# Optimization experiments

Hardware: AMD Instinct MI355X
Metric: run time of the kernel (lower is better)

## Reference

```python
import jax, jax.numpy as jnp
import numpy as np

B, C, T, H, W = 2, 128, 16, 64, 64
MAX_STEPS = 12
EXP = 2  # ReactionMLP expansion
LN_EPS = 1e-5


def setup_inputs() -> dict:
    key = jax.random.key(0)
    ks = jax.random.split(key, 12)
    s = 0.05
    u = jax.random.normal(ks[0], (B, C, T, H, W), jnp.float32)
    # Linear weights stored as (in, out); torch uses y = x @ W.T + b
    Wg = jax.random.normal(ks[1], (C, C), jnp.float32) * s
    bg = jnp.zeros((C,), jnp.float32)
    Wv = jax.random.normal(ks[2], (C, C), jnp.float32) * s
    bv = jnp.zeros((C,), jnp.float32)
    W1 = jax.random.normal(ks[3], (C, C * EXP), jnp.float32) * s
    b1 = jnp.zeros((C * EXP,), jnp.float32)
    W2 = jax.random.normal(ks[4], (C * EXP, C), jnp.float32) * s
    b2 = jnp.zeros((C,), jnp.float32)
    gamma = jnp.ones((C,), jnp.float32)
    beta = jnp.zeros((C,), jnp.float32)
    alpha = jnp.float32(0.1)
    log_dt = jnp.log(jnp.float32(0.1))
    return {"u": u, "Wg": Wg, "bg": bg, "Wv": Wv, "bv": bv,
            "W1": W1, "b1": b1, "W2": W2, "b2": b2,
            "gamma": gamma, "beta": beta, "alpha": alpha, "log_dt": log_dt}


def _layernorm(x, g, b):
    m = x.mean(-1, keepdims=True)
    xc = x - m
    v = (xc * xc).mean(-1, keepdims=True)
    return xc * jax.lax.rsqrt(v + LN_EPS) * g + b


def reference(u, Wg, bg, Wv, bv, W1, b1, W2, b2, gamma, beta, alpha, log_dt):
    Bv, Cv, Tv, Hv, Wd = u.shape
    N = Tv * Hv * Wd
    u_flat = u.transpose(0, 2, 3, 4, 1).reshape(Bv, N, Cv)  # (B, N, C)
    h0 = jnp.zeros((Bv, Cv), u.dtype)
    a = jax.nn.softplus(alpha)
    dt = jnp.clip(jnp.exp(log_dt), 0.01, 0.2)

    def step(carry, _):
        uf, h, u_prev = carry
        # Reaction MLP (per-position), torch GELU is erf-based
        react = jax.nn.gelu(uf @ W1 + b1, approximate=False) @ W2 + b2
        # Memory pump on pooled features
        u_pooled = uf.mean(axis=1)  # (B, C)
        h = h + jax.nn.sigmoid(u_pooled @ Wg + bg) * jnp.tanh(u_pooled @ Wv + bv)
        # use_pde=False -> diffusion term is zero
        du = react + a * h[:, None, :]
        u_new = _layernorm(uf + dt * du, gamma, beta)
        turb = jnp.abs(u_new - u_prev).mean() / (jnp.abs(u_prev).mean() + 1e-8)
        return (u_new, h, u_new), turb

    (uf, _, _), turbs = jax.lax.scan(step, (u_flat, h0, u_flat), None, length=MAX_STEPS)
    u_out = uf.reshape(Bv, Tv, Hv, Wd, Cv).transpose(0, 4, 1, 2, 3)
    return u_out, turbs.mean()
```

## Files before the change

### kernel.cpp

```cpp
#include <hip/hip_runtime.h>

#define NPOS 65536
#define NSTEPS 12

#define USTATE_OFF  0ull
#define STATS_OFF   67108864ull
#define H_OFF       (STATS_OFF + 128ull)
#define POOLED0_OFF (H_OFF + 2048ull)
#define PARTS_OFF   (POOLED0_OFF + 1024ull)
#define WS_END      (PARTS_OFF + 98304ull)
#define ZERO_BYTES  (WS_END - STATS_OFF)

#define L_W    0
#define L_Y1   16384
#define L_X    32832
#define L_POOL 36928
#define L_AH   37184
#define L_RED  37440
#define L_SCR  39488
#define L_TOT  39504
#define SMEM_BYTES (L_TOT * 4)

__device__ __forceinline__ float gelu_erf(float x) {
  return 0.5f * x * (1.0f + erff(x * 0.70710678118654752440f));
}

__global__ __launch_bounds__(256) void pool0_kernel(const float* __restrict__ u,
                                                    float* __restrict__ pooled0,
                                                    float* __restrict__ stats) {
  int bc = blockIdx.x;
  const float4* src = (const float4*)(u + (size_t)bc * NPOS);
  int t = threadIdx.x;
  float s = 0.f, sa = 0.f;
#pragma unroll 4
  for (int i = 0; i < 64; ++i) {
    float4 v = src[i * 256 + t];
    s += v.x + v.y + v.z + v.w;
    sa += fabsf(v.x) + fabsf(v.y) + fabsf(v.z) + fabsf(v.w);
  }
  for (int o = 1; o < 64; o <<= 1) { s += __shfl_xor(s, o, 64); sa += __shfl_xor(sa, o, 64); }
  __shared__ float sc[8];
  int lane = t & 63, w = t >> 6;
  if (lane == 0) { sc[w] = s; sc[4 + w] = sa; }
  __syncthreads();
  if (t == 0) {
    pooled0[bc] = sc[0] + sc[1] + sc[2] + sc[3];
    atomicAdd(&stats[0], sc[4] + sc[5] + sc[6] + sc[7]);
  }
}

template <int MODE>
__global__ __launch_bounds__(512)
void fused_step(const float* __restrict__ u_in, float* __restrict__ ustate,
                float* __restrict__ d_out,
                const float* __restrict__ gamma, const float* __restrict__ beta,
                const float* __restrict__ W1, const float* __restrict__ b1,
                const float* __restrict__ W2,
                const float* __restrict__ Wg, const float* __restrict__ bg,
                const float* __restrict__ Wv, const float* __restrict__ bv,
                const float* __restrict__ b2,
                const float* __restrict__ alpha_p, const float* __restrict__ logdt_p,
                float* __restrict__ h_g, const float* __restrict__ pooled0,
                float* __restrict__ parts, float* __restrict__ stats, int step) {
  extern __shared__ float sm[];
  float* sW   = sm + L_W;
  float* sY   = sm + L_Y1;
  float* sX   = sm + L_X;
  float* sPool = sm + L_POOL;
  float* sAh  = sm + L_AH;
  float* sRed = sm + L_RED;
  float* sScr = sm + L_SCR;

  int t = threadIdx.x;
  int bid = blockIdx.x;

  {
    int zb = (step + 2) % 3;
    for (int i = t; i < 8192; i += 512) parts[zb * 8192 + i] = 0.f;
  }
  if (t < 256) {
    float ps;
    if (MODE == 0) {
      ps = pooled0[t];
    } else {
      const float* pp = parts + (size_t)(step % 3) * 8192;
      ps = 0.f;
#pragma unroll
      for (int s = 0; s < 32; ++s) ps += pp[s * 256 + t];
    }
    sPool[t] = ps * (1.0f / 65536.0f);
  }
  __syncthreads();
  if (t < 256) {
    int bb = t >> 7, c = t & 127;
    float gi = bg[c], vi = bv[c];
    const float* pl = sPool + bb * 128;
    for (int k = 0; k < 128; ++k) {
      float pv = pl[k];
      gi = fmaf(pv, Wg[k * 128 + c], gi);
      vi = fmaf(pv, Wv[k * 128 + c], vi);
    }
    float sg = 1.0f / (1.0f + expf(-gi));
    float th = tanhf(vi);
    int hb = step & 1;
    float hn = h_g[hb * 256 + t] + sg * th;
    if (MODE < 2 && bid == 0) h_g[(hb ^ 1) * 256 + t] = hn;
    float aa = log1pf(expf(alpha_p[0]));
    sAh[t] = aa * hn + b2[c];
  }
  __syncthreads();

  float dtv = fminf(fmaxf(expf(logdt_p[0]), 0.01f), 0.2f);
  int b = bid >> 8;
  int og = t & 63, pgw = t >> 6;
  int og2 = t & 31, pg2 = t >> 5;
  int lane = t & 63, wv = t >> 6;

  float preg[4] = {0.f, 0.f, 0.f, 0.f};
  float acc_ad = 0.f, acc_au = 0.f;

  float4* sWf = (float4*)sW;
  const float4* W1f = (const float4*)W1;
  const float4* W2f = (const float4*)W2;

  for (int tt = 0; tt < 4; ++tt) {
    int pos0 = bid * 256 + tt * 64;
    int n0 = pos0 & (NPOS - 1);

    float a1[4][8];
#pragma unroll
    for (int i = 0; i < 4; ++i)
#pragma unroll
      for (int k = 0; k < 8; ++k) a1[i][k] = 0.f;

    for (int h = 0; h < 2; ++h) {
      __syncthreads();
#pragma unroll
      for (int it = 0; it < 8; ++it) {
        int idx = it * 512 + t;
        sWf[idx] = W1f[(size_t)(h * 64 + (idx >> 6)) * 64 + (idx & 63)];
      }
      if (MODE == 0) {
#pragma unroll
        for (int it = 0; it < 8; ++it) {
          int idx = it * 512 + t;
          int pp_ = idx & 63, cc = idx >> 6;
          sX[pp_ * 64 + cc] =
              u_in[(size_t)(b * 128 + h * 64 + cc) * NPOS + (size_t)(n0 + pp_)];
        }
      } else {
        float4* sXf = (float4*)sX;
        const float4* us4 = (const float4*)ustate;
#pragma unroll
        for (int it = 0; it < 2; ++it) {
          int idx = it * 512 + t;
          int pp_ = idx >> 4, c4 = idx & 15;
          sXf[pp_ * 16 + c4] = us4[(size_t)(pos0 + pp_) * 32 + h * 16 + c4];
        }
      }
      __syncthreads();
      const float4* Wc = (const float4*)sW;
      for (int cc = 0; cc < 64; ++cc) {
        float4 w = Wc[cc * 64 + og];
        float xv[8];
#pragma unroll
        for (int k = 0; k < 8; ++k) xv[k] = sX[(pgw * 8 + k) * 64 + cc];
#pragma unroll
        for (int k = 0; k < 8; ++k) {
          a1[0][k] = fmaf(w.x, xv[k], a1[0][k]);
          a1[1][k] = fmaf(w.y, xv[k], a1[1][k]);
          a1[2][k] = fmaf(w.z, xv[k], a1[2][k]);
          a1[3][k] = fmaf(w.w, xv[k], a1[3][k]);
        }
      }
    }
    {
      float bb1[4];
#pragma unroll
      for (int i = 0; i < 4; ++i) bb1[i] = b1[og * 4 + i];
#pragma unroll
      for (int k = 0; k < 8; ++k)
#pragma unroll
        for (int i = 0; i < 4; ++i)
          sY[(pgw * 8 + k) * 257 + og * 4 + i] = gelu_erf(a1[i][k] + bb1[i]);
    }

    float a2[4][4];
#pragma unroll
    for (int i = 0; i < 4; ++i)
#pragma unroll
      for (int k = 0; k < 4; ++k) a2[i][k] = 0.f;

    for (int h = 0; h < 2; ++h) {
      __syncthreads();
#pragma unroll
      for (int it = 0; it < 8; ++it) {
        int idx = it * 512 + t;
        sWf[idx] = W2f[(size_t)(h * 128 + (idx >> 5)) * 32 + (idx & 31)];
      }
      __syncthreads();
      const float4* Wc = (const float4*)sW;
      for (int cc = 0; cc < 128; ++cc) {
        float4 w = Wc[cc * 32 + og2];
        float yv[4];
#pragma unroll
        for (int k = 0; k < 4; ++k) yv[k] = sY[(pg2 * 4 + k) * 257 + h * 128 + cc];
#pragma unroll
        for (int k = 0; k < 4; ++k) {
          a2[0][k] = fmaf(w.x, yv[k], a2[0][k]);
          a2[1][k] = fmaf(w.y, yv[k], a2[1][k]);
          a2[2][k] = fmaf(w.z, yv[k], a2[2][k]);
          a2[3][k] = fmaf(w.w, yv[k], a2[3][k]);
        }
      }
    }

    int ch0 = og2 * 4;
    float ahv[4], gmv[4], btv[4];
#pragma unroll
    for (int i = 0; i < 4; ++i) {
      ahv[i] = sAh[b * 128 + ch0 + i];
      gmv[i] = gamma[ch0 + i];
      btv[i] = beta[ch0 + i];
    }
#pragma unroll
    for (int k = 0; k < 4; ++k) {
      int pos = pos0 + pg2 * 4 + k;
      int n = pos & (NPOS - 1);
      float uf[4];
      if (MODE == 0) {
#pragma unroll
        for (int i = 0; i < 4; ++i)
          uf[i] = u_in[(size_t)(b * 128 + ch0 + i) * NPOS + n];
      } else {
        float4 q = *(const float4*)(ustate + (size_t)pos * 128 + ch0);
        uf[0] = q.x; uf[1] = q.y; uf[2] = q.z; uf[3] = q.w;
      }
      float x[4], s1 = 0.f, s2 = 0.f;
#pragma unroll
      for (int i = 0; i < 4; ++i) {
        float du = a2[i][k] + ahv[i];
        x[i] = uf[i] + dtv * du;
        s1 += x[i]; s2 += x[i] * x[i];
      }
      for (int o = 1; o < 32; o <<= 1) {
        s1 += __shfl_xor(s1, o, 64);
        s2 += __shfl_xor(s2, o, 64);
      }
      float mean = s1 * (1.0f / 128.0f);
      float var = s2 * (1.0f / 128.0f) - mean * mean;
      float rstd = rsqrtf(var + 1e-5f);
      float un[4];
#pragma unroll
      for (int i = 0; i < 4; ++i) un[i] = (x[i] - mean) * rstd * gmv[i] + btv[i];
      if (MODE == 2) {
#pragma unroll
        for (int i = 0; i < 4; ++i)
          d_out[(size_t)(b * 128 + ch0 + i) * NPOS + n] = un[i];
      } else {
        *(float4*)(ustate + (size_t)pos * 128 + ch0) =
            make_float4(un[0], un[1], un[2], un[3]);
      }
#pragma unroll
      for (int i = 0; i < 4; ++i) {
        acc_ad += fabsf(un[i] - uf[i]);
        acc_au += fabsf(un[i]);
        preg[i] += un[i];
      }
    }
  }

  for (int o = 1; o < 64; o <<= 1) {
    acc_ad += __shfl_xor(acc_ad, o, 64);
    acc_au += __shfl_xor(acc_au, o, 64);
  }
  if (lane == 0) { sScr[wv] = acc_ad; sScr[8 + wv] = acc_au; }
#pragma unroll
  for (int i = 0; i < 4; ++i) sRed[t * 4 + i] = preg[i];
  __syncthreads();
  if (t == 0) {
    float ad = 0.f, au = 0.f;
#pragma unroll
    for (int w = 0; w < 8; ++w) { ad += sScr[w]; au += sScr[8 + w]; }
    atomicAdd(&stats[17 + step], ad);
    atomicAdd(&stats[1 + step], au);
  }
  if (MODE < 2 && t < 128) {
    float v = 0.f;
#pragma unroll
    for (int pg = 0; pg < 16; ++pg) v += sRed[(pg * 32 + (t >> 2)) * 4 + (t & 3)];
    atomicAdd(&parts[(size_t)((step + 1) % 3) * 8192 + (bid & 31) * 256 + b * 128 + t], v);
  }
}

__global__ void finalize_kernel(const float* __restrict__ stats, float* __restrict__ out) {
  if (threadIdx.x == 0 && blockIdx.x == 0) {
    const float inv = 1.0f / 16777216.0f;
    float tm = 0.f;
#pragma unroll
    for (int k = 1; k <= 12; ++k)
      tm += (stats[16 + k] * inv) / (stats[k - 1] * inv + 1e-8f);
    out[16777216] = tm * (1.0f / 12.0f);
  }
}

extern "C" void kernel_launch(void* const* d_in, const int* in_sizes, int n_in,
                              void* d_out, int out_size, void* d_ws, size_t ws_size,
                              hipStream_t stream) {
  const float* u     = (const float*)d_in[0];
  const float* Wg    = (const float*)d_in[1];
  const float* bg    = (const float*)d_in[2];
  const float* Wv    = (const float*)d_in[3];
  const float* bv    = (const float*)d_in[4];
  const float* W1    = (const float*)d_in[5];
  const float* b1    = (const float*)d_in[6];
  const float* W2    = (const float*)d_in[7];
  const float* b2    = (const float*)d_in[8];
  const float* gamma = (const float*)d_in[9];
  const float* beta  = (const float*)d_in[10];
  const float* alpha = (const float*)d_in[11];
  const float* logdt = (const float*)d_in[12];
  float* out = (float*)d_out;
  char* ws = (char*)d_ws;
  if (ws_size < WS_END) return;

  float* ustate  = (float*)(ws + USTATE_OFF);
  float* stats   = (float*)(ws + STATS_OFF);
  float* h_g     = (float*)(ws + H_OFF);
  float* pooled0 = (float*)(ws + POOLED0_OFF);
  float* parts   = (float*)(ws + PARTS_OFF);

  hipFuncSetAttribute(reinterpret_cast<const void*>(&fused_step<0>),
                      hipFuncAttributeMaxDynamicSharedMemorySize, SMEM_BYTES);
  hipFuncSetAttribute(reinterpret_cast<const void*>(&fused_step<1>),
                      hipFuncAttributeMaxDynamicSharedMemorySize, SMEM_BYTES);
  hipFuncSetAttribute(reinterpret_cast<const void*>(&fused_step<2>),
                      hipFuncAttributeMaxDynamicSharedMemorySize, SMEM_BYTES);

  hipMemsetAsync(ws + STATS_OFF, 0, ZERO_BYTES, stream);
  pool0_kernel<<<256, 256, 0, stream>>>(u, pooled0, stats);

  for (int step = 0; step < NSTEPS; ++step) {
    if (step == 0)
      fused_step<0><<<512, 512, SMEM_BYTES, stream>>>(
          u, ustate, out, gamma, beta, W1, b1, W2, Wg, bg, Wv, bv, b2,
          alpha, logdt, h_g, pooled0, parts, stats, step);
    else if (step == NSTEPS - 1)
      fused_step<2><<<512, 512, SMEM_BYTES, stream>>>(
          u, ustate, out, gamma, beta, W1, b1, W2, Wg, bg, Wv, bv, b2,
          alpha, logdt, h_g, pooled0, parts, stats, step);
    else
      fused_step<1><<<512, 512, SMEM_BYTES, stream>>>(
          u, ustate, out, gamma, beta, W1, b1, W2, Wg, bg, Wv, bv, b2,
          alpha, logdt, h_g, pooled0, parts, stats, step);
  }
  finalize_kernel<<<1, 64, 0, stream>>>(stats, out);
}
```

Baseline: 4.056 ms.

## Use bf16x3 split MFMA for reaction MLP with pre-packed weights

Replaces the scalar FP32 FMA matmuls with bf16 MFMA 16x16x32 instructions, splitting each FP32 operand into high and low bf16 parts and using three products to keep near-FP32 accuracy. A prep kernel packs W1/W2 into the MFMA fragment layout once per launch. The high halves are held in LDS and the low halves are read from global memory. Each wave now processes 32-position tiles independently, passing GELU outputs between lanes with shuffles instead of an LDS round-trip. Block count drops to 256, and the large LDS footprint limits occupancy.

New measurement: 6.330 ms. +56.1%, slower.

```diff
diff --git a/kernel.cpp b/kernel.cpp
--- a/kernel.cpp
+++ b/kernel.cpp
@@ -1,28 +1,82 @@
 #include <hip/hip_runtime.h>
 
+#define C_DIM 128
 #define NPOS 65536
 #define NSTEPS 12
+#define TILE_P 32
+#define FBLOCKS 256
+#define FTHREADS 512
+#define TOTAL_WAVES 2048
+#define TILES_PER_WAVE 2
+
+typedef short short8 __attribute__((ext_vector_type(8)));
+typedef float floatx4 __attribute__((ext_vector_type(4)));
 
 #define USTATE_OFF  0ull
-#define STATS_OFF   67108864ull
+#define PW_OFF      67108864ull
+#define STATS_OFF   (PW_OFF + 262144ull)
 #define H_OFF       (STATS_OFF + 128ull)
 #define POOLED0_OFF (H_OFF + 2048ull)
 #define PARTS_OFF   (POOLED0_OFF + 1024ull)
 #define WS_END      (PARTS_OFF + 98304ull)
 #define ZERO_BYTES  (WS_END - STATS_OFF)
 
-#define L_W    0
-#define L_Y1   16384
-#define L_X    32832
-#define L_POOL 36928
-#define L_AH   37184
-#define L_RED  37440
-#define L_SCR  39488
-#define L_TOT  39504
-#define SMEM_BYTES (L_TOT * 4)
-
+#define SM_PW1   0
+#define SM_PW2   65536
+#define SM_GAMMA 131072
+#define SM_BETA  131584
+#define SM_B1    132096
+#define SM_AH    133120
+#define SM_POOL  134144
+#define SM_PACC  135168
+#define SM_SCR   136192
+#define SMEM_BYTES 136320
+
+__device__ __forceinline__ unsigned short f2bf(float f) {
+  unsigned u = __builtin_bit_cast(unsigned, f);
+  u += 0x7fffu + ((u >> 16) & 1u);
+  return (unsigned short)(u >> 16);
+}
+__device__ __forceinline__ void split2(float a, float b, unsigned& hw, unsigned& lw) {
+  unsigned ha = (unsigned)f2bf(a), hb = (unsigned)f2bf(b);
+  float ra = a - __builtin_bit_cast(float, ha << 16);
+  float rb = b - __builtin_bit_cast(float, hb << 16);
+  hw = ha | (hb << 16);
+  lw = (unsigned)f2bf(ra) | ((unsigned)f2bf(rb) << 16);
+}
 __device__ __forceinline__ float gelu_erf(float x) {
   return 0.5f * x * (1.0f + erff(x * 0.70710678118654752440f));
+}
+__device__ __forceinline__ floatx4 mfma16(short8 a, short8 b, floatx4 c) {
+  return __builtin_amdgcn_mfma_f32_16x16x32_bf16(a, b, c, 0, 0, 0);
+}
+
+__global__ __launch_bounds__(256) void prep_weights(const float* __restrict__ W1,
+                                                    const float* __restrict__ W2,
+                                                    int4* __restrict__ pw) {
+  int t = blockIdx.x * 256 + threadIdx.x;
+  float v[8];
+  if (t < 4096) {
+    int f = t >> 6, l = t & 63;
+    int ct = f >> 2, kt = f & 3;
+    int row = ct * 16 + (l & 15);
+    int c = kt * 32 + (l >> 4) * 8;
+#pragma unroll
+    for (int j = 0; j < 8; ++j) v[j] = W1[(c + j) * 256 + row];
+  } else {
+    int t2 = t - 4096;
+    int f = t2 >> 6, l = t2 & 63;
+    int ct2 = f >> 3, kt2 = f & 7;
+    int row = ct2 * 16 + (l & 15);
+    int c = kt2 * 32 + (l >> 4) * 8;
+#pragma unroll
+    for (int j = 0; j < 8; ++j) v[j] = W2[(c + j) * 128 + row];
+  }
+  unsigned hw[4], lw[4];
+#pragma unroll
+  for (int jj = 0; jj < 4; ++jj) split2(v[2 * jj], v[2 * jj + 1], hw[jj], lw[jj]);
+  pw[t]        = make_int4((int)hw[0], (int)hw[1], (int)hw[2], (int)hw[3]);
+  pw[8192 + t] = make_int4((int)lw[0], (int)lw[1], (int)lw[2], (int)lw[3]);
 }
 
 __global__ __launch_bounds__(256) void pool0_kernel(const float* __restrict__ u,
@@ -50,51 +104,55 @@
 }
 
 template <int MODE>
-__global__ __launch_bounds__(512)
+__global__ __launch_bounds__(FTHREADS, 2)
 void fused_step(const float* __restrict__ u_in, float* __restrict__ ustate,
-                float* __restrict__ d_out,
+                float* __restrict__ d_out, const uint4* __restrict__ pw_g,
                 const float* __restrict__ gamma, const float* __restrict__ beta,
-                const float* __restrict__ W1, const float* __restrict__ b1,
-                const float* __restrict__ W2,
+                const float* __restrict__ b1, const float* __restrict__ b2,
                 const float* __restrict__ Wg, const float* __restrict__ bg,
                 const float* __restrict__ Wv, const float* __restrict__ bv,
-                const float* __restrict__ b2,
                 const float* __restrict__ alpha_p, const float* __restrict__ logdt_p,
                 float* __restrict__ h_g, const float* __restrict__ pooled0,
                 float* __restrict__ parts, float* __restrict__ stats, int step) {
-  extern __shared__ float sm[];
-  float* sW   = sm + L_W;
-  float* sY   = sm + L_Y1;
-  float* sX   = sm + L_X;
-  float* sPool = sm + L_POOL;
-  float* sAh  = sm + L_AH;
-  float* sRed = sm + L_RED;
-  float* sScr = sm + L_SCR;
-
-  int t = threadIdx.x;
-  int bid = blockIdx.x;
-
+  extern __shared__ char smem[];
+  uint4* s_pw    = (uint4*)(smem + SM_PW1);
+  float* s_gamma = (float*)(smem + SM_GAMMA);
+  float* s_beta  = (float*)(smem + SM_BETA);
+  float* s_b1    = (float*)(smem + SM_B1);
+  float* s_ah    = (float*)(smem + SM_AH);
+  float* s_pool  = (float*)(smem + SM_POOL);
+  float* s_pacc  = (float*)(smem + SM_PACC);
+  float* s_scr   = (float*)(smem + SM_SCR);
+
+  int tid = threadIdx.x;
+
+#pragma unroll
+  for (int i = 0; i < 16; ++i) s_pw[i * FTHREADS + tid] = pw_g[i * FTHREADS + tid];
+  if (tid < 128) { s_gamma[tid] = gamma[tid]; s_beta[tid] = beta[tid]; }
+  if (tid >= 128 && tid < 384) s_b1[tid - 128] = b1[tid - 128];
+  if (tid < 256) s_pacc[tid] = 0.f;
   {
     int zb = (step + 2) % 3;
-    for (int i = t; i < 8192; i += 512) parts[zb * 8192 + i] = 0.f;
-  }
-  if (t < 256) {
+#pragma unroll
+    for (int i = tid; i < 8192; i += FTHREADS) parts[zb * 8192 + i] = 0.f;
+  }
+  if (tid < 256) {
     float ps;
     if (MODE == 0) {
-      ps = pooled0[t];
+      ps = pooled0[tid];
     } else {
       const float* pp = parts + (size_t)(step % 3) * 8192;
       ps = 0.f;
 #pragma unroll
-      for (int s = 0; s < 32; ++s) ps += pp[s * 256 + t];
+      for (int s = 0; s < 32; ++s) ps += pp[s * 256 + tid];
     }
-    sPool[t] = ps * (1.0f / 65536.0f);
+    s_pool[tid] = ps * (1.0f / 65536.0f);
   }
   __syncthreads();
-  if (t < 256) {
-    int bb = t >> 7, c = t & 127;
+  if (tid < 256) {
+    int b = tid >> 7, c = tid & 127;
     float gi = bg[c], vi = bv[c];
-    const float* pl = sPool + bb * 128;
+    const float* pl = s_pool + b * 128;
     for (int k = 0; k < 128; ++k) {
       float pv = pl[k];
       gi = fmaf(pv, Wg[k * 128 + c], gi);
@@ -103,169 +161,186 @@
     float sg = 1.0f / (1.0f + expf(-gi));
     float th = tanhf(vi);
     int hb = step & 1;
-    float hn = h_g[hb * 256 + t] + sg * th;
-    if (MODE < 2 && bid == 0) h_g[(hb ^ 1) * 256 + t] = hn;
+    float hn = h_g[hb * 256 + tid] + sg * th;
+    if (MODE < 2 && blockIdx.x == 0) h_g[(hb ^ 1) * 256 + tid] = hn;
     float aa = log1pf(expf(alpha_p[0]));
-    sAh[t] = aa * hn + b2[c];
+    s_ah[tid] = aa * hn + b2[c];
   }
   __syncthreads();
 
   float dtv = fminf(fmaxf(expf(logdt_p[0]), 0.01f), 0.2f);
-  int b = bid >> 8;
-  int og = t & 63, pgw = t >> 6;
-  int og2 = t & 31, pg2 = t >> 5;
-  int lane = t & 63, wv = t >> 6;
-
-  float preg[4] = {0.f, 0.f, 0.f, 0.f};
+  int lane = tid & 63, wv = tid >> 6;
+  int p = lane & 15, g = lane >> 4;
+  int wid = blockIdx.x * 8 + wv;
   float acc_ad = 0.f, acc_au = 0.f;
 
-  float4* sWf = (float4*)sW;
-  const float4* W1f = (const float4*)W1;
-  const float4* W2f = (const float4*)W2;
-
-  for (int tt = 0; tt < 4; ++tt) {
-    int pos0 = bid * 256 + tt * 64;
-    int n0 = pos0 & (NPOS - 1);
-
-    float a1[4][8];
-#pragma unroll
-    for (int i = 0; i < 4; ++i)
-#pragma unroll
-      for (int k = 0; k < 8; ++k) a1[i][k] = 0.f;
-
-    for (int h = 0; h < 2; ++h) {
-      __syncthreads();
-#pragma unroll
-      for (int it = 0; it < 8; ++it) {
-        int idx = it * 512 + t;
-        sWf[idx] = W1f[(size_t)(h * 64 + (idx >> 6)) * 64 + (idx & 63)];
-      }
-      if (MODE == 0) {
-#pragma unroll
-        for (int it = 0; it < 8; ++it) {
-          int idx = it * 512 + t;
-          int pp_ = idx & 63, cc = idx >> 6;
-          sX[pp_ * 64 + cc] =
-              u_in[(size_t)(b * 128 + h * 64 + cc) * NPOS + (size_t)(n0 + pp_)];
-        }
-      } else {
-        float4* sXf = (float4*)sX;
-        const float4* us4 = (const float4*)ustate;
-#pragma unroll
-        for (int it = 0; it < 2; ++it) {
-          int idx = it * 512 + t;
-          int pp_ = idx >> 4, c4 = idx & 15;
-          sXf[pp_ * 16 + c4] = us4[(size_t)(pos0 + pp_) * 32 + h * 16 + c4];
-        }
-      }
-      __syncthreads();
-      const float4* Wc = (const float4*)sW;
-      for (int cc = 0; cc < 64; ++cc) {
-        float4 w = Wc[cc * 64 + og];
+  for (int it = 0; it < TILES_PER_WAVE; ++it) {
+    int tile = wid + it * TOTAL_WAVES;
+    int p0 = tile * TILE_P;
+    int b = p0 >> 16;
+    float preg[8][4];
+#pragma unroll
+    for (int c8 = 0; c8 < 8; ++c8)
+#pragma unroll
+      for (int r = 0; r < 4; ++r) preg[c8][r] = 0.f;
+
+#pragma unroll
+    for (int pt = 0; pt < 2; ++pt) {
+      int pos = p0 + pt * 16 + p;
+      int n = pos & (NPOS - 1);
+
+      short8 bxh[4], bxl[4];
+#pragma unroll
+      for (int kt = 0; kt < 4; ++kt) {
         float xv[8];
-#pragma unroll
-        for (int k = 0; k < 8; ++k) xv[k] = sX[(pgw * 8 + k) * 64 + cc];
-#pragma unroll
-        for (int k = 0; k < 8; ++k) {
-          a1[0][k] = fmaf(w.x, xv[k], a1[0][k]);
-          a1[1][k] = fmaf(w.y, xv[k], a1[1][k]);
-          a1[2][k] = fmaf(w.z, xv[k], a1[2][k]);
-          a1[3][k] = fmaf(w.w, xv[k], a1[3][k]);
-        }
-      }
-    }
-    {
-      float bb1[4];
-#pragma unroll
-      for (int i = 0; i < 4; ++i) bb1[i] = b1[og * 4 + i];
-#pragma unroll
-      for (int k = 0; k < 8; ++k)
-#pragma unroll
-        for (int i = 0; i < 4; ++i)
-          sY[(pgw * 8 + k) * 257 + og * 4 + i] = gelu_erf(a1[i][k] + bb1[i]);
-    }
-
-    float a2[4][4];
-#pragma unroll
-    for (int i = 0; i < 4; ++i)
-#pragma unroll
-      for (int k = 0; k < 4; ++k) a2[i][k] = 0.f;
-
-    for (int h = 0; h < 2; ++h) {
-      __syncthreads();
-#pragma unroll
-      for (int it = 0; it < 8; ++it) {
-        int idx = it * 512 + t;
-        sWf[idx] = W2f[(size_t)(h * 128 + (idx >> 5)) * 32 + (idx & 31)];
-      }
-      __syncthreads();
-      const float4* Wc = (const float4*)sW;
-      for (int cc = 0; cc < 128; ++cc) {
-        float4 w = Wc[cc * 32 + og2];
-        float yv[4];
-#pragma unroll
-        for (int k = 0; k < 4; ++k) yv[k] = sY[(pg2 * 4 + k) * 257 + h * 128 + cc];
-#pragma unroll
-        for (int k = 0; k < 4; ++k) {
-          a2[0][k] = fmaf(w.x, yv[k], a2[0][k]);
-          a2[1][k] = fmaf(w.y, yv[k], a2[1][k]);
-          a2[2][k] = fmaf(w.z, yv[k], a2[2][k]);
-          a2[3][k] = fmaf(w.w, yv[k], a2[3][k]);
-        }
-      }
-    }
-
-    int ch0 = og2 * 4;
-    float ahv[4], gmv[4], btv[4];
-#pragma unroll
-    for (int i = 0; i < 4; ++i) {
-      ahv[i] = sAh[b * 128 + ch0 + i];
-      gmv[i] = gamma[ch0 + i];
-      btv[i] = beta[ch0 + i];
-    }
-#pragma unroll
-    for (int k = 0; k < 4; ++k) {
-      int pos = pos0 + pg2 * 4 + k;
-      int n = pos & (NPOS - 1);
-      float uf[4];
-      if (MODE == 0) {
-#pragma unroll
-        for (int i = 0; i < 4; ++i)
-          uf[i] = u_in[(size_t)(b * 128 + ch0 + i) * NPOS + n];
-      } else {
-        float4 q = *(const float4*)(ustate + (size_t)pos * 128 + ch0);
-        uf[0] = q.x; uf[1] = q.y; uf[2] = q.z; uf[3] = q.w;
-      }
-      float x[4], s1 = 0.f, s2 = 0.f;
-#pragma unroll
-      for (int i = 0; i < 4; ++i) {
-        float du = a2[i][k] + ahv[i];
-        x[i] = uf[i] + dtv * du;
-        s1 += x[i]; s2 += x[i] * x[i];
-      }
-      for (int o = 1; o < 32; o <<= 1) {
-        s1 += __shfl_xor(s1, o, 64);
-        s2 += __shfl_xor(s2, o, 64);
-      }
+        if (MODE == 0) {
+          size_t base = ((size_t)(b * C_DIM + kt * 32 + g * 8)) * NPOS + n;
+#pragma unroll
+          for (int j = 0; j < 8; ++j) xv[j] = u_in[base + (size_t)j * NPOS];
+        } else {
+          const float* src = ustate + (size_t)pos * C_DIM + kt * 32 + g * 8;
+          float4 qa = *(const float4*)src;
+          float4 qb = *(const float4*)(src + 4);
+          xv[0] = qa.x; xv[1] = qa.y; xv[2] = qa.z; xv[3] = qa.w;
+          xv[4] = qb.x; xv[5] = qb.y; xv[6] = qb.z; xv[7] = qb.w;
+        }
+        unsigned hw[4], lw[4];
+#pragma unroll
+        for (int jj = 0; jj < 4; ++jj) split2(xv[2 * jj], xv[2 * jj + 1], hw[jj], lw[jj]);
+        bxh[kt] = __builtin_bit_cast(short8, make_int4((int)hw[0], (int)hw[1], (int)hw[2], (int)hw[3]));
+        bxl[kt] = __builtin_bit_cast(short8, make_int4((int)lw[0], (int)lw[1], (int)lw[2], (int)lw[3]));
+      }
+
+      floatx4 acc1[16];
+#pragma unroll
+      for (int ct = 0; ct < 16; ++ct) acc1[ct] = (floatx4){0.f, 0.f, 0.f, 0.f};
+#pragma unroll
+      for (int ct = 0; ct < 16; ++ct) {
+#pragma unroll
+        for (int kt = 0; kt < 4; ++kt) {
+          int f = (ct * 4 + kt) * 64 + lane;
+          short8 wh = __builtin_bit_cast(short8, s_pw[f]);
+          short8 wl = __builtin_bit_cast(short8, pw_g[8192 + f]);
+          acc1[ct] = mfma16(wh, bxh[kt], acc1[ct]);
+          acc1[ct] = mfma16(wh, bxl[kt], acc1[ct]);
+          acc1[ct] = mfma16(wl, bxh[kt], acc1[ct]);
+        }
+      }
+
+      floatx4 acc2[8];
+#pragma unroll
+      for (int ct2 = 0; ct2 < 8; ++ct2) acc2[ct2] = (floatx4){0.f, 0.f, 0.f, 0.f};
+      int srcA = p + ((g & 1) << 5);
+      int srcB = srcA + 16;
+      bool hisel = (g >> 1) != 0;
+#pragma unroll
+      for (int kt2 = 0; kt2 < 8; ++kt2) {
+        int pkh[2][2], pkl[2][2];
+#pragma unroll
+        for (int cc = 0; cc < 2; ++cc) {
+          int ct = 2 * kt2 + cc;
+          float4 b1v = *(const float4*)(s_b1 + ct * 16 + g * 4);
+          float v0 = gelu_erf(acc1[ct][0] + b1v.x);
+          float v1 = gelu_erf(acc1[ct][1] + b1v.y);
+          float v2 = gelu_erf(acc1[ct][2] + b1v.z);
+          float v3 = gelu_erf(acc1[ct][3] + b1v.w);
+          unsigned h0, l0, h1, l1;
+          split2(v0, v1, h0, l0);
+          split2(v2, v3, h1, l1);
+          pkh[cc][0] = (int)h0; pkh[cc][1] = (int)h1;
+          pkl[cc][0] = (int)l0; pkl[cc][1] = (int)l1;
+        }
+        int d0a = __shfl(pkh[0][0], srcA, 64), d0b = __shfl(pkh[1][0], srcA, 64);
+        int d1a = __shfl(pkh[0][1], srcA, 64), d1b = __shfl(pkh[1][1], srcA, 64);
+        int d2a = __shfl(pkh[0][0], srcB, 64), d2b = __shfl(pkh[1][0], srcB, 64);
+        int d3a = __shfl(pkh[0][1], srcB, 64), d3b = __shfl(pkh[1][1], srcB, 64);
+        int4 qh = make_int4(hisel ? d0b : d0a, hisel ? d1b : d1a,
+                            hisel ? d2b : d2a, hisel ? d3b : d3a);
+        int e0a = __shfl(pkl[0][0], srcA, 64), e0b = __shfl(pkl[1][0], srcA, 64);
+        int e1a = __shfl(pkl[0][1], srcA, 64), e1b = __shfl(pkl[1][1], srcA, 64);
+        int e2a = __shfl(pkl[0][0], srcB, 64), e2b = __shfl(pkl[1][0], srcB, 64);
+        int e3a = __shfl(pkl[0][1], srcB, 64), e3b = __shfl(pkl[1][1], srcB, 64);
+        int4 ql = make_int4(hisel ? e0b : e0a, hisel ? e1b : e1a,
+                            hisel ? e2b : e2a, hisel ? e3b : e3a);
+        short8 bfh = __builtin_bit_cast(short8, qh);
+        short8 bfl = __builtin_bit_cast(short8, ql);
+#pragma unroll
+        for (int ct2 = 0; ct2 < 8; ++ct2) {
+          int f = (ct2 * 8 + kt2) * 64 + lane;
+          short8 wh = __builtin_bit_cast(short8, s_pw[4096 + f]);
+          short8 wl = __builtin_bit_cast(short8, pw_g[12288 + f]);
+          acc2[ct2] = mfma16(wh, bfh, acc2[ct2]);
+          acc2[ct2] = mfma16(wh, bfl, acc2[ct2]);
+          acc2[ct2] = mfma16(wl, bfh, acc2[ct2]);
+        }
+      }
+
+      float xr[8][4], ufr[8][4];
+      float s1 = 0.f, s2 = 0.f;
+#pragma unroll
+      for (int ct2 = 0; ct2 < 8; ++ct2) {
+        int ch0 = ct2 * 16 + g * 4;
+        float uf[4];
+        if (MODE == 0) {
+          size_t base = ((size_t)(b * C_DIM + ch0)) * NPOS + n;
+          uf[0] = u_in[base]; uf[1] = u_in[base + NPOS];
+          uf[2] = u_in[base + 2 * (size_t)NPOS]; uf[3] = u_in[base + 3 * (size_t)NPOS];
+        } else {
+          float4 q = *(const float4*)(ustate + (size_t)pos * C_DIM + ch0);
+          uf[0] = q.x; uf[1] = q.y; uf[2] = q.z; uf[3] = q.w;
+        }
+        float4 ahv = *(const float4*)(s_ah + b * 128 + ch0);
+#pragma unroll
+        for (int r = 0; r < 4; ++r) {
+          float ah = (r == 0) ? ahv.x : (r == 1) ? ahv.y : (r == 2) ? ahv.z : ahv.w;
+          float du = acc2[ct2][r] + ah;
+          float x = uf[r] + dtv * du;
+          xr[ct2][r] = x; ufr[ct2][r] = uf[r];
+          s1 += x; s2 += x * x;
+        }
+      }
+      s1 += __shfl_xor(s1, 16, 64); s1 += __shfl_xor(s1, 32, 64);
+      s2 += __shfl_xor(s2, 16, 64); s2 += __shfl_xor(s2, 32, 64);
       float mean = s1 * (1.0f / 128.0f);
       float var = s2 * (1.0f / 128.0f) - mean * mean;
       float rstd = rsqrtf(var + 1e-5f);
-      float un[4];
-#pragma unroll
-      for (int i = 0; i < 4; ++i) un[i] = (x[i] - mean) * rstd * gmv[i] + btv[i];
-      if (MODE == 2) {
-#pragma unroll
-        for (int i = 0; i < 4; ++i)
-          d_out[(size_t)(b * 128 + ch0 + i) * NPOS + n] = un[i];
-      } else {
-        *(float4*)(ustate + (size_t)pos * 128 + ch0) =
-            make_float4(un[0], un[1], un[2], un[3]);
-      }
-#pragma unroll
-      for (int i = 0; i < 4; ++i) {
-        acc_ad += fabsf(un[i] - uf[i]);
-        acc_au += fabsf(un[i]);
-        preg[i] += un[i];
+#pragma unroll
+      for (int ct2 = 0; ct2 < 8; ++ct2) {
+        int ch0 = ct2 * 16 + g * 4;
+        float4 gm = *(const float4*)(s_gamma + ch0);
+        float4 bt = *(const float4*)(s_beta + ch0);
+        float un[4];
+        un[0] = (xr[ct2][0] - mean) * rstd * gm.x + bt.x;
+        un[1] = (xr[ct2][1] - mean) * rstd * gm.y + bt.y;
+        un[2] = (xr[ct2][2] - mean) * rstd * gm.z + bt.z;
+        un[3] = (xr[ct2][3] - mean) * rstd * gm.w + bt.w;
+        if (MODE == 2) {
+          size_t base = ((size_t)(b * C_DIM + ch0)) * NPOS + n;
+          d_out[base] = un[0]; d_out[base + NPOS] = un[1];
+          d_out[base + 2 * (size_t)NPOS] = un[2]; d_out[base + 3 * (size_t)NPOS] = un[3];
+        } else {
+          *(float4*)(ustate + (size_t)pos * C_DIM + ch0) =
+              make_float4(un[0], un[1], un[2], un[3]);
+        }
+#pragma unroll
+        for (int r = 0; r < 4; ++r) {
+          acc_ad += fabsf(un[r] - ufr[ct2][r]);
+          acc_au += fabsf(un[r]);
+          if (MODE < 2) preg[ct2][r] += un[r];
+        }
+      }
+    }
+
+    if (MODE < 2) {
+#pragma unroll
+      for (int ct2 = 0; ct2 < 8; ++ct2) {
+#pragma unroll
+        for (int r = 0; r < 4; ++r) {
+          float v = preg[ct2][r];
+          v += __shfl_xor(v, 1, 64); v += __shfl_xor(v, 2, 64);
+          v += __shfl_xor(v, 4, 64); v += __shfl_xor(v, 8, 64);
+          if (p == 0) unsafeAtomicAdd(&s_pacc[b * 128 + ct2 * 16 + g * 4 + r], v);
+        }
       }
     }
   }
@@ -274,22 +349,19 @@
     acc_ad += __shfl_xor(acc_ad, o, 64);
     acc_au += __shfl_xor(acc_au, o, 64);
   }
-  if (lane == 0) { sScr[wv] = acc_ad; sScr[8 + wv] = acc_au; }
-#pragma unroll
-  for (int i = 0; i < 4; ++i) sRed[t * 4 + i] = preg[i];
+  if (lane == 0) { s_scr[wv * 2] = acc_ad; s_scr[wv * 2 + 1] = acc_au; }
   __syncthreads();
-  if (t == 0) {
+  if (tid == 0) {
     float ad = 0.f, au = 0.f;
 #pragma unroll
-    for (int w = 0; w < 8; ++w) { ad += sScr[w]; au += sScr[8 + w]; }
+    for (int w = 0; w < 8; ++w) { ad += s_scr[w * 2]; au += s_scr[w * 2 + 1]; }
     atomicAdd(&stats[17 + step], ad);
-    atomicAdd(&stats[1 + step], au);
-  }
-  if (MODE < 2 && t < 128) {
-    float v = 0.f;
-#pragma unroll
-    for (int pg = 0; pg < 16; ++pg) v += sRed[(pg * 32 + (t >> 2)) * 4 + (t & 3)];
-    atomicAdd(&parts[(size_t)((step + 1) % 3) * 8192 + (bid & 31) * 256 + b * 128 + t], v);
+    atomicAdd(&stats[step + 1], au);
+  }
+  __syncthreads();
+  if (MODE < 2 && tid < 256) {
+    atomicAdd(&parts[(size_t)((step + 1) % 3) * 8192 + (blockIdx.x & 31) * 256 + tid],
+              s_pacc[tid]);
   }
 }
 
@@ -325,6 +397,7 @@
   if (ws_size < WS_END) return;
 
   float* ustate  = (float*)(ws + USTATE_OFF);
+  int4*  pw      = (int4*)(ws + PW_OFF);
   float* stats   = (float*)(ws + STATS_OFF);
   float* h_g     = (float*)(ws + H_OFF);
   float* pooled0 = (float*)(ws + POOLED0_OFF);
@@ -338,20 +411,21 @@
                       hipFuncAttributeMaxDynamicSharedMemorySize, SMEM_BYTES);
 
   hipMemsetAsync(ws + STATS_OFF, 0, ZERO_BYTES, stream);
+  prep_weights<<<32, 256, 0, stream>>>(W1, W2, pw);
   pool0_kernel<<<256, 256, 0, stream>>>(u, pooled0, stats);
 
   for (int step = 0; step < NSTEPS; ++step) {
     if (step == 0)
-      fused_step<0><<<512, 512, SMEM_BYTES, stream>>>(
-          u, ustate, out, gamma, beta, W1, b1, W2, Wg, bg, Wv, bv, b2,
+      fused_step<0><<<FBLOCKS, FTHREADS, SMEM_BYTES, stream>>>(
+          u, ustate, out, (const uint4*)pw, gamma, beta, b1, b2, Wg, bg, Wv, bv,
           alpha, logdt, h_g, pooled0, parts, stats, step);
     else if (step == NSTEPS - 1)
-      fused_step<2><<<512, 512, SMEM_BYTES, stream>>>(
-          u, ustate, out, gamma, beta, W1, b1, W2, Wg, bg, Wv, bv, b2,
+      fused_step<2><<<FBLOCKS, FTHREADS, SMEM_BYTES, stream>>>(
+          u, ustate, out, (const uint4*)pw, gamma, beta, b1, b2, Wg, bg, Wv, bv,
           alpha, logdt, h_g, pooled0, parts, stats, step);
     else
-      fused_step<1><<<512, 512, SMEM_BYTES, stream>>>(
-          u, ustate, out, gamma, beta, W1, b1, W2, Wg, bg, Wv, bv, b2,
+      fused_step<1><<<FBLOCKS, FTHREADS, SMEM_BYTES, stream>>>(
+          u, ustate, out, (const uint4*)pw, gamma, beta, b1, b2, Wg, bg, Wv, bv,
           alpha, logdt, h_g, pooled0, parts, stats, step);
   }
   finalize_kernel<<<1, 64, 0, stream>>>(stats, out);
```
